# Kernel tuning notes

Measured on AMD Instinct MI355X. Metric: run time of the kernel, lower is better.

The kernel has to match this reference:

```python
import jax, jax.numpy as jnp
import numpy as np

N_NODES, N_EDGES, NNZ = 10000, 4000, 30000
IN_CH, HEADS, OUT_CH = 128, 2, 64


def _scale2_pattern(node, edge, num_nodes, num_edges):
    """Sparsity pattern of H @ (H^T H) where H is the node x edge incidence.
    Mirrors torch.sparse.mm + coalesce + (values > 0) mask (pattern only,
    since all values are positive sums of ones)."""
    # unique incidence pattern (coalesce)
    uk = np.unique(node.astype(np.int64) * num_edges + edge.astype(np.int64))
    n_u, e_u = uk // num_edges, uk % num_edges
    # --- stage 1: pattern of H^T H = edge pairs sharing a node ---
    order = np.argsort(n_u, kind="stable")
    ns, es = n_u[order], e_u[order]
    _, starts, cnts = np.unique(ns, return_index=True, return_counts=True)
    cpe = np.repeat(cnts, cnts)          # group size per sorted entry
    gpe = np.repeat(starts, cnts)        # group start per sorted entry
    tot = int(cpe.sum())
    within = np.arange(tot) - np.repeat(np.cumsum(cpe) - cpe, cpe)
    pe = np.repeat(es, cpe)
    pep = es[np.repeat(gpe, cpe) + within]
    pk = np.unique(pe * num_edges + pep)
    pe, pep = pk // num_edges, pk % num_edges
    # --- stage 2: pattern of H @ (H^T H) ---
    po = np.argsort(pe, kind="stable")
    pe_s, pep_s = pe[po], pep[po]
    cnt_e = np.bincount(pe_s, minlength=num_edges)
    ptr = np.concatenate([np.zeros(1, np.int64), np.cumsum(cnt_e)])
    c2 = cnt_e[e_u]
    tot2 = int(c2.sum())
    within2 = np.arange(tot2) - np.repeat(np.cumsum(c2) - c2, c2)
    v2 = np.repeat(n_u, c2)
    ep2 = pep_s[ptr[e_u].repeat(c2) + within2]
    k2 = np.unique(v2 * num_edges + ep2)
    return k2 // num_edges, k2 % num_edges


def setup_inputs() -> dict:
    rng = np.random.default_rng(0)
    node1 = rng.integers(0, N_NODES, NNZ).astype(np.int64)
    edge1 = rng.integers(0, N_EDGES, NNZ).astype(np.int64)
    node2, edge2 = _scale2_pattern(node1, edge1, N_NODES, N_EDGES)

    key = jax.random.key(0)
    k = jax.random.split(key, 4)
    HO = HEADS * OUT_CH
    xav1 = (2.0 / (IN_CH + HO)) ** 0.5
    xavo = (2.0 / (HO + OUT_CH)) ** 0.5
    return {
        "x": jax.random.normal(k[0], (N_NODES, IN_CH), jnp.float32),
        "hyperedge_index1": jnp.asarray(np.stack([node1, edge1]), jnp.int32),
        "hyperedge_index2": jnp.asarray(np.stack([node2, edge2]), jnp.int32),
        "W1": jax.random.normal(k[1], (HO, IN_CH), jnp.float32) * xav1,
        "b1": jnp.zeros((HO,), jnp.float32),
        "W2": jax.random.normal(k[2], (HO, IN_CH), jnp.float32) * xav1,
        "b2": jnp.zeros((HO,), jnp.float32),
        "Wout": jax.random.normal(k[3], (OUT_CH, HO), jnp.float32) * xavo,
        "bout": jnp.zeros((OUT_CH,), jnp.float32),
        "num_edges": N_EDGES,
    }


def _hconv(x, W, b, node_idx, edge_idx, num_edges):
    num_nodes = x.shape[0]
    xt = x @ W.T + b                                  # [N, H*O]
    g = xt[node_idx]                                  # [nnz, H*O] gather
    esum = jax.ops.segment_sum(g, edge_idx, num_segments=num_edges)
    cnt = jax.ops.segment_sum(jnp.ones(edge_idx.shape, xt.dtype), edge_idx,
                              num_segments=num_edges)
    emean = esum / jnp.maximum(cnt, 1.0)[:, None]     # scatter_mean (0 if empty)
    return jax.ops.segment_sum(emean[edge_idx], node_idx,
                               num_segments=num_nodes)  # scatter_add


def reference(x, hyperedge_index1, hyperedge_index2, W1, b1, W2, b2, Wout, bout,
              num_edges):
    o1 = _hconv(x, W1, b1, hyperedge_index1[0], hyperedge_index1[1], num_edges)
    o2 = _hconv(x, W2, b2, hyperedge_index2[0], hyperedge_index2[1], num_edges)
    o = 0.5 * (o1 + o2)                               # mean over 2 scales
    return o @ Wout.T + bout                          # output_proj
```

## Files before the change

kernel.cpp:

```cpp
#include <hip/hip_runtime.h>
#include <hip/hip_bf16.h>

#define N_NODES 10000
#define N_EDGES 4000
#define IN_CH   128
#define HOC     128
#define OUT_CH  64
#define CHUNK   16384

#define G_GEMM  625
#define G_NPTR  40

__device__ __forceinline__ float bf2f(unsigned short u) {
    union { unsigned int i; float f; } v;
    v.i = ((unsigned int)u) << 16;
    return v.f;
}
__device__ __forceinline__ unsigned short f2bfu(float f) {
    union { __hip_bfloat16 h; unsigned short u; } v;
    v.h = __float2bfloat16(f);
    return v.u;
}

__device__ __forceinline__ void load8(const void* base, size_t eoff, int isf32,
                                      float o[8]) {
    if (isf32) {
        const float4* q = (const float4*)((const float*)base + eoff);
        float4 a = q[0], b = q[1];
        o[0]=a.x; o[1]=a.y; o[2]=a.z; o[3]=a.w;
        o[4]=b.x; o[5]=b.y; o[6]=b.z; o[7]=b.w;
    } else {
        uint4 v = *(const uint4*)((const unsigned short*)base + eoff);
        const unsigned short* pv = (const unsigned short*)&v;
#pragma unroll
        for (int q = 0; q < 8; q++) o[q] = bf2f(pv[q]);
    }
}

__device__ __forceinline__ float loadS(const void* base, int i, int isf32) {
    return isf32 ? ((const float*)base)[i] : bf2f(((const unsigned short*)base)[i]);
}

__device__ __forceinline__ int probe_isf32(const unsigned int* __restrict__ x) {
    const int lane = threadIdx.x & 63;
    unsigned int w0 = x[lane * 2], w1 = x[lane * 2 + 1];
    int h = 0, z = 0;
    {
        unsigned int lo = w0 & 0xFFFFu;
        if (lo == 0u) z++; else if (((lo >> 7) & 0xFF) >= 0x90u) h++;
        lo = w1 & 0xFFFFu;
        if (lo == 0u) z++; else if (((lo >> 7) & 0xFF) >= 0x90u) h++;
    }
    unsigned long long bh = __ballot(h > 0);
    unsigned long long bz = __ballot(z == 2);
    return (__popcll(bh) > 8 || __popcll(bz) > 50) ? 1 : 0;
}

__device__ __forceinline__ void add4(float acc[4], uint2 u) {
    acc[0] += bf2f((unsigned short)(u.x & 0xFFFFu));
    acc[1] += bf2f((unsigned short)(u.x >> 16));
    acc[2] += bf2f((unsigned short)(u.y & 0xFFFFu));
    acc[3] += bf2f((unsigned short)(u.y >> 16));
}

__global__ __launch_bounds__(256) void weff_zero(
    const void* __restrict__ Wout,
    const void* __restrict__ W1, const void* __restrict__ b1,
    const void* __restrict__ W2, const void* __restrict__ b2,
    float* __restrict__ weff1, float* __restrict__ beff1,
    float* __restrict__ weff2, float* __restrict__ beff2,
    int* __restrict__ cntz, int* __restrict__ fillz,
    const unsigned int* __restrict__ xprobe)
{
    const int b = blockIdx.x;
    if (b == 4) {
        for (int t = threadIdx.x; t < 18000; t += 256) cntz[t] = 0;
        for (int t = threadIdx.x; t < 14000; t += 256) fillz[t] = 0;
        return;
    }
    __shared__ float wsh[64][IN_CH];
    const int isf32 = probe_isf32(xprobe);

    if (b == 5) {
        float* bsh = &wsh[0][0];
        const int t = threadIdx.x;
        {
            const int s = t >> 7, h = t & 127;
            bsh[t] = loadS(s ? b2 : b1, h, isf32);
        }
        __syncthreads();
        if (t < 128) {
            const int s = t >> 6, o = t & 63;
            float a = 0.f;
#pragma unroll 4
            for (int r = 0; r < 16; r++) {
                float v[8];
                load8(Wout, (size_t)o * 128 + r * 8, isf32, v);
#pragma unroll
                for (int q = 0; q < 8; q++) a += v[q] * bsh[s * 128 + r * 8 + q];
            }
            (s ? beff2 : beff1)[o] = 0.5f * a;
        }
        return;
    }

    const int s  = b >> 1;
    const int oh = b & 1;
    const void* Ws = s ? W2 : W1;
    float* outW = s ? weff2 : weff1;
    const int o  = oh * 32 + (threadIdx.x >> 3);
    const int i0 = (threadIdx.x & 7) * 16;
    float acc[16];
#pragma unroll
    for (int k = 0; k < 16; k++) acc[k] = 0.f;

    for (int pass = 0; pass < 2; pass++) {
        if (pass) __syncthreads();
        for (int r = 0; r < 4; r++) {
            int idx = r * 2048 + threadIdx.x * 8;
            float v[8];
            load8(Ws, (size_t)pass * 8192 + idx, isf32, v);
            float* d = &wsh[0][0] + idx;
#pragma unroll
            for (int q = 0; q < 8; q++) d[q] = v[q];
        }
        float wrow[64];
#pragma unroll
        for (int r = 0; r < 8; r++) {
            float v[8];
            load8(Wout, (size_t)o * 128 + pass * 64 + r * 8, isf32, v);
#pragma unroll
            for (int q = 0; q < 8; q++) wrow[r * 8 + q] = v[q];
        }
        __syncthreads();
#pragma unroll 4
        for (int h = 0; h < 64; h++) {
            const float wo = wrow[h];
            const float* wr = &wsh[h][i0];
#pragma unroll
            for (int k = 0; k < 16; k++) acc[k] += wo * wr[k];
        }
    }
#pragma unroll
    for (int k = 0; k < 16; k++)
        outW[o * 128 + i0 + k] = 0.5f * acc[k];
}

__global__ __launch_bounds__(256) void prep(
    const void* __restrict__ x,
    const float* __restrict__ weff1, const float* __restrict__ beff1,
    const float* __restrict__ weff2, const float* __restrict__ beff2,
    unsigned short* __restrict__ xtP1b, unsigned short* __restrict__ xtP2b,
    const int* __restrict__ idx1, int nnz1,
    const int* __restrict__ idx2, int nnz2,
    int* __restrict__ nptr,
    int* __restrict__ bh, int* __restrict__ cnt2,
    int* __restrict__ cnt1e, int* __restrict__ cnt1n, int nblk)
{
    __shared__ __align__(16) char smem[40000];
    int b = blockIdx.x;

    if (b < nblk) {
        int* h = (int*)smem;
        for (int t = threadIdx.x; t < N_EDGES; t += 256) h[t] = 0;
        __syncthreads();
        const int lo = b * CHUNK;
        const int hi = min(nnz2, lo + CHUNK);
        for (int i = lo + threadIdx.x; i < hi; i += 256)
            atomicAdd(&h[idx2[nnz2 + i]], 1);
        __syncthreads();
        int* dst = bh + (size_t)b * N_EDGES;
        for (int t = threadIdx.x; t < N_EDGES; t += 256) {
            int v = h[t];
            dst[t] = v;
            if (v) atomicAdd(&cnt2[t], v);
        }
        return;
    }
    b -= nblk;

    if (b < 8) {
        const int isEdge = b < 4;
        const int bid = isEdge ? b : (b - 4);
        const int nb = isEdge ? N_EDGES : N_NODES;
        const int* src = isEdge ? (idx1 + nnz1) : idx1;
        int* dst = isEdge ? cnt1e : cnt1n;
        int* h = (int*)smem;
        for (int t = threadIdx.x; t < nb; t += 256) h[t] = 0;
        __syncthreads();
        for (int i = bid * 256 + threadIdx.x; i < nnz1; i += 4 * 256)
            atomicAdd(&h[src[i]], 1);
        __syncthreads();
        for (int t = threadIdx.x; t < nb; t += 256) {
            int v = h[t];
            if (v) atomicAdd(&dst[t], v);
        }
        return;
    }
    b -= 8;

    if (b < G_GEMM) {
        const int isf32 = probe_isf32((const unsigned int*)x);
        float (*xs)[IN_CH] = (float (*)[IN_CH])smem;
        const int n0 = b * 16;
        {
            float v[8];
            load8(x, (size_t)n0 * IN_CH + (size_t)threadIdx.x * 8, isf32, v);
            float* dst = &xs[0][0] + threadIdx.x * 8;
#pragma unroll
            for (int q = 0; q < 8; q++) dst[q] = v[q];
        }
        __syncthreads();

        const int g   = threadIdx.x >> 7;
        const int sel = (threadIdx.x >> 6) & 1;
        const int j   = threadIdx.x & 63;
        const float* WE = sel ? weff2 : weff1;
        const float* BE = sel ? beff2 : beff1;
        unsigned short* xtP = sel ? xtP2b : xtP1b;

        float acc[8];
#pragma unroll
        for (int m = 0; m < 8; m++) acc[m] = 0.f;

        const float4* Wr = (const float4*)(WE + (size_t)j * 128);
        for (int kk = 0; kk < 16; kk++) {
            float4 a = Wr[kk * 2], c = Wr[kk * 2 + 1];
            float w[8] = {a.x, a.y, a.z, a.w, c.x, c.y, c.z, c.w};
#pragma unroll
            for (int m = 0; m < 8; m++) {
                const float* xr = &xs[g * 8 + m][kk * 8];
                acc[m] += xr[0]*w[0] + xr[1]*w[1] + xr[2]*w[2] + xr[3]*w[3]
                        + xr[4]*w[4] + xr[5]*w[5] + xr[6]*w[6] + xr[7]*w[7];
            }
        }
        const float bias = BE[j];
#pragma unroll
        for (int m = 0; m < 8; m++)
            xtP[(size_t)(n0 + g * 8 + m) * 64 + j] = f2bfu(acc[m] + bias);
        return;
    }
    b -= G_GEMM;

    {
        int n = b * 256 + threadIdx.x;
        if (n > N_NODES) return;
        int lo = 0, hi = nnz2;
        while (lo < hi) { int mid = (lo + hi) >> 1; if (idx2[mid] < n) lo = mid + 1; else hi = mid; }
        nptr[n] = lo;
    }
}

__global__ __launch_bounds__(256) void scans3(
    const int* __restrict__ cnt2, int* __restrict__ ptr2,
    const int* __restrict__ cnt1e, int* __restrict__ ptr1e,
    const int* __restrict__ cnt1n, int* __restrict__ ptr1n)
{
    const int* cnt; int* ptr; int nb;
    if (blockIdx.x == 0)      { cnt = cnt2;  ptr = ptr2;  nb = N_EDGES; }
    else if (blockIdx.x == 1) { cnt = cnt1e; ptr = ptr1e; nb = N_EDGES; }
    else                      { cnt = cnt1n; ptr = ptr1n; nb = N_NODES; }
    __shared__ int part[256];
    const int t = threadIdx.x;
    const int K = (nb + 255) >> 8;
    const int base = t * K;
    int s = 0;
    for (int q = 0; q < K; q++) {
        int i = base + q;
        s += (i < nb) ? cnt[i] : 0;
    }
    part[t] = s;
    __syncthreads();
    for (int d = 1; d < 256; d <<= 1) {
        int v = (t >= d) ? part[t - d] : 0;
        __syncthreads();
        part[t] += v;
        __syncthreads();
    }
    int run = part[t] - s;
    for (int q = 0; q < K; q++) {
        int i = base + q;
        if (i < nb) { ptr[i] = run; run += cnt[i]; }
    }
    if (t == 255) ptr[nb] = part[255];
}

__global__ __launch_bounds__(256) void sb_fb(
    const int* __restrict__ ptr2, int* __restrict__ bh, int nblk,
    const int* __restrict__ idx1, int nnz1,
    const int* __restrict__ ptr1e, int* __restrict__ fill1e,
    unsigned short* __restrict__ nodelist1,
    const int* __restrict__ ptr1n, int* __restrict__ fill1n,
    unsigned short* __restrict__ edgelist1)
{
    int b = blockIdx.x;
    if (b < 16) {
        int e = b * 256 + threadIdx.x;
        if (e >= N_EDGES) return;
        int run = ptr2[e];
        int k = 0;
        for (; k + 8 <= nblk; k += 8) {
            int v[8];
#pragma unroll
            for (int q = 0; q < 8; q++)
                v[q] = bh[(size_t)(k + q) * N_EDGES + e];
#pragma unroll
            for (int q = 0; q < 8; q++) {
                bh[(size_t)(k + q) * N_EDGES + e] = run;
                run += v[q];
            }
        }
        for (; k < nblk; k++) {
            int i = k * N_EDGES + e;
            int t = bh[i];
            bh[i] = run;
            run += t;
        }
        return;
    }
    b -= 16;
    int i = b * 256 + threadIdx.x;
    if (i >= nnz1) return;
    int n = idx1[i];
    int e = idx1[nnz1 + i];
    int se = atomicAdd(&fill1e[e], 1);
    nodelist1[ptr1e[e] + se] = (unsigned short)n;
    int sn = atomicAdd(&fill1n[n], 1);
    edgelist1[ptr1n[n] + sn] = (unsigned short)e;
}

__global__ __launch_bounds__(1024) void place_entries(
    const int* __restrict__ idx, int nnz, const int* __restrict__ bh,
    unsigned short* __restrict__ nodelist)
{
    __shared__ int lh[N_EDGES];
    for (int t = threadIdx.x; t < N_EDGES; t += 1024) lh[t] = 0;
    __syncthreads();
    const int b = blockIdx.x;
    const int lo = b * CHUNK;
    const int hi = min(nnz, lo + CHUNK);
    const int* bhb = bh + (size_t)b * N_EDGES;
    for (int i = lo + threadIdx.x; i < hi; i += 1024) {
        int n = idx[i];
        int e = idx[nnz + i];
        int s = atomicAdd(&lh[e], 1);
        nodelist[bhb[e] + s] = (unsigned short)n;
    }
}

__global__ __launch_bounds__(256) void edge_gather(
    const unsigned short* __restrict__ nodelist2, const int* __restrict__ ptr2,
    const unsigned int* __restrict__ xtP2u, unsigned int* __restrict__ emean2b,
    const unsigned short* __restrict__ nodelist1, const int* __restrict__ ptr1e,
    const unsigned int* __restrict__ xtP1u, unsigned int* __restrict__ emean1b)
{
    int b = blockIdx.x;
    if (b < 1000) {
        const int lane = threadIdx.x & 63;
        const int sub  = lane >> 4;
        const int ch4  = lane & 15;
        const int e = b * 4 + (threadIdx.x >> 6);
        const int lo = ptr2[e], hi = ptr2[e + 1];
        const uint2* src2 = (const uint2*)xtP2u;
        float acc[4] = {0.f, 0.f, 0.f, 0.f};
        int i = lo;
        for (; i + 32 <= hi; i += 32) {
            int n[8]; uint2 u[8];
#pragma unroll
            for (int q = 0; q < 8; q++) n[q] = nodelist2[i + 4 * q + sub];
#pragma unroll
            for (int q = 0; q < 8; q++) u[q] = src2[(size_t)n[q] * 16 + ch4];
#pragma unroll
            for (int q = 0; q < 8; q++) add4(acc, u[q]);
        }
        for (; i < hi; i += 4) {
            if (i + sub < hi) {
                int n0 = nodelist2[i + sub];
                add4(acc, src2[(size_t)n0 * 16 + ch4]);
            }
        }
#pragma unroll
        for (int q = 0; q < 4; q++) {
            acc[q] += __shfl_xor(acc[q], 16);
            acc[q] += __shfl_xor(acc[q], 32);
        }
        if (sub == 0) {
            const float inv = 1.f / fmaxf((float)(hi - lo), 1.f);
            uint2 o;
            o.x = ((unsigned int)f2bfu(acc[1] * inv) << 16) | f2bfu(acc[0] * inv);
            o.y = ((unsigned int)f2bfu(acc[3] * inv) << 16) | f2bfu(acc[2] * inv);
            ((uint2*)emean2b)[(size_t)e * 16 + ch4] = o;
        }
        return;
    }
    b -= 1000;
    {
        const int lane = threadIdx.x & 31;
        const int e = b * 8 + (threadIdx.x >> 5);
        const int lo = ptr1e[e], hi = ptr1e[e + 1];
        float accx = 0.f, accy = 0.f;
        for (int base = lo; base < hi; base += 32) {
            const int m = min(32, hi - base);
            int vl = (base + lane < hi) ? (int)nodelist1[base + lane] : 0;
            int t = 0;
            for (; t + 7 < m; t += 8) {
                int nn[8]; unsigned int uu[8];
#pragma unroll
                for (int q = 0; q < 8; q++) nn[q] = __shfl(vl, t + q, 32);
#pragma unroll
                for (int q = 0; q < 8; q++) uu[q] = xtP1u[nn[q] * 32 + lane];
#pragma unroll
                for (int q = 0; q < 8; q++) {
                    accx += bf2f((unsigned short)(uu[q] & 0xFFFFu));
                    accy += bf2f((unsigned short)(uu[q] >> 16));
                }
            }
            for (; t < m; t++) {
                int n = __shfl(vl, t, 32);
                unsigned int u = xtP1u[n * 32 + lane];
                accx += bf2f((unsigned short)(u & 0xFFFFu));
                accy += bf2f((unsigned short)(u >> 16));
            }
        }
        const float inv = 1.f / fmaxf((float)(hi - lo), 1.f);
        emean1b[e * 32 + lane] =
            ((unsigned int)f2bfu(accy * inv) << 16) | f2bfu(accx * inv);
    }
}

__global__ __launch_bounds__(256) void node_final(
    const int* __restrict__ vals2, const int* __restrict__ nptr,
    const unsigned int* __restrict__ emean2b,
    const unsigned short* __restrict__ edgelist1, const int* __restrict__ ptr1n,
    const unsigned int* __restrict__ emean1b,
    const void* __restrict__ bout, void* __restrict__ out,
    const unsigned int* __restrict__ xprobe)
{
    const int isf32 = probe_isf32(xprobe);
    const int lane = threadIdx.x & 63;
    const int sub  = lane >> 4;
    const int ch4  = lane & 15;
    const int n = blockIdx.x * 4 + (threadIdx.x >> 6);
    float acc[4] = {0.f, 0.f, 0.f, 0.f};

    {
        const int lo = nptr[n], hi = nptr[n + 1];
        const uint2* src = (const uint2*)emean2b;
        int i = lo;
        for (; i + 32 <= hi; i += 32) {
            int e[8]; uint2 u[8];
#pragma unroll
            for (int q = 0; q < 8; q++) e[q] = vals2[i + 4 * q + sub];
#pragma unroll
            for (int q = 0; q < 8; q++) u[q] = src[(size_t)e[q] * 16 + ch4];
#pragma unroll
            for (int q = 0; q < 8; q++) add4(acc, u[q]);
        }
        for (; i < hi; i += 4) {
            if (i + sub < hi)
                add4(acc, src[(size_t)vals2[i + sub] * 16 + ch4]);
        }
    }
    {
        const int lo = ptr1n[n], hi = ptr1n[n + 1];
        const uint2* src = (const uint2*)emean1b;
        int i = lo;
        for (; i + 32 <= hi; i += 32) {
            int e[8]; uint2 u[8];
#pragma unroll
            for (int q = 0; q < 8; q++) e[q] = edgelist1[i + 4 * q + sub];
#pragma unroll
            for (int q = 0; q < 8; q++) u[q] = src[(size_t)e[q] * 16 + ch4];
#pragma unroll
            for (int q = 0; q < 8; q++) add4(acc, u[q]);
        }
        for (; i < hi; i += 4) {
            if (i + sub < hi)
                add4(acc, src[(size_t)edgelist1[i + sub] * 16 + ch4]);
        }
    }
#pragma unroll
    for (int q = 0; q < 4; q++) {
        acc[q] += __shfl_xor(acc[q], 16);
        acc[q] += __shfl_xor(acc[q], 32);
    }
    if (sub == 0) {
        float r[4];
#pragma unroll
        for (int q = 0; q < 4; q++)
            r[q] = acc[q] + loadS(bout, ch4 * 4 + q, isf32);
        if (isf32) {
            ((float4*)out)[(size_t)n * 16 + ch4] =
                make_float4(r[0], r[1], r[2], r[3]);
        } else {
            uint2 o;
            o.x = ((unsigned int)f2bfu(r[1]) << 16) | f2bfu(r[0]);
            o.y = ((unsigned int)f2bfu(r[3]) << 16) | f2bfu(r[2]);
            ((uint2*)out)[(size_t)n * 16 + ch4] = o;
        }
    }
}

extern "C" void kernel_launch(void* const* d_in, const int* in_sizes, int n_in,
                              void* d_out, int out_size, void* d_ws, size_t ws_size,
                              hipStream_t stream)
{
    const void* x  = d_in[0];
    const int* idx1 = (const int*)d_in[1];
    const int* idx2 = (const int*)d_in[2];
    const void* W1 = d_in[3];
    const void* b1 = d_in[4];
    const void* W2 = d_in[5];
    const void* b2 = d_in[6];
    const void* Wo = d_in[7];
    const void* bo = d_in[8];

    const int nnz1 = in_sizes[1] / 2;
    const int nnz2 = in_sizes[2] / 2;
    const int nblk = (nnz2 + CHUNK - 1) / CHUNK;

    float* ws = (float*)d_ws;
    unsigned short* xtP1b = (unsigned short*)ws;
    unsigned int*   xtP1u = (unsigned int*)xtP1b;
    unsigned short* xtP2b = (unsigned short*)(ws + 320000);
    unsigned int*   xtP2u = (unsigned int*)xtP2b;
    int*   fill1e = (int*)(ws + 1280000);
    int*   fill1n = (int*)(ws + 1284000);
    int* cnt2  = (int*)(ws + 1550000);
    int* cnt1e = (int*)(ws + 1554000);
    int* cnt1n = (int*)(ws + 1558000);
    int* ptr2  = (int*)(ws + 1568000);
    int* ptr1e = (int*)(ws + 1572004);
    int* ptr1n = (int*)(ws + 1576008);
    int* nptr  = (int*)(ws + 1586012);
    float* weff1 = ws + 1596016;
    float* weff2 = ws + 1604208;
    float* beff1 = ws + 1612400;
    float* beff2 = ws + 1612464;
    unsigned int* emean2b = (unsigned int*)(ws + 1612528);
    unsigned int* emean1b = (unsigned int*)(ws + 1740528);
    unsigned short* nodelist2 = (unsigned short*)(ws + 1868528);
    const size_t nl2u = ((size_t)nnz2 + 1) / 2;
    unsigned short* nodelist1 = (unsigned short*)(ws + 1868528 + nl2u);
    const size_t nl1u = ((size_t)nnz1 + 1) / 2;
    unsigned short* edgelist1 = (unsigned short*)(ws + 1868528 + nl2u + nl1u);
    const size_t bh_off = (1868528 + nl2u + 2 * nl1u + 7) & ~(size_t)7;
    int* bh = (int*)(ws + bh_off);

    weff_zero<<<6, 256, 0, stream>>>(Wo, W1, b1, W2, b2,
                                     weff1, beff1, weff2, beff2,
                                     cnt2, fill1e, (const unsigned int*)x);

    prep<<<nblk + 8 + G_GEMM + G_NPTR, 256, 0, stream>>>(
        x, weff1, beff1, weff2, beff2, xtP1b, xtP2b,
        idx1, nnz1, idx2, nnz2,
        nptr, bh, cnt2, cnt1e, cnt1n, nblk);

    scans3<<<3, 256, 0, stream>>>(cnt2, ptr2, cnt1e, ptr1e, cnt1n, ptr1n);

    sb_fb<<<16 + (nnz1 + 255) / 256, 256, 0, stream>>>(
        ptr2, bh, nblk, idx1, nnz1, ptr1e, fill1e, nodelist1,
        ptr1n, fill1n, edgelist1);

    place_entries<<<nblk, 1024, 0, stream>>>(idx2, nnz2, bh, nodelist2);

    edge_gather<<<1000 + N_EDGES / 8, 256, 0, stream>>>(
        nodelist2, ptr2, xtP2u, emean2b,
        nodelist1, ptr1e, xtP1u, emean1b);

    node_final<<<N_NODES / 4, 256, 0, stream>>>(
        idx2 + nnz2, nptr, emean2b, edgelist1, ptr1n, emean1b,
        bo, d_out, (const unsigned int*)x);
}
```

Baseline: 198.5 us.

## Replace per-block histogram CSR build with global atomic fill for scale-2

The scale-2 CSR construction no longer stores per-chunk edge histograms, scans them per edge and places entries in a separate kernel. Entries are now scattered directly with global atomic counters per edge, fused into the same launch as the scale-1 fill. This drops one kernel launch, the histogram writes and the column-wise scan. In exchange it uses many global atomics on 4000 counters for a large nnz2, which risks contention, and the node order inside each edge list becomes nondeterministic.

After: 220.1 us. +10.9%, slower.

```diff
diff --git a/kernel.cpp b/kernel.cpp
--- a/kernel.cpp
+++ b/kernel.cpp
@@ -4,8 +4,6 @@
 #define N_NODES 10000
 #define N_EDGES 4000
 #define IN_CH   128
-#define HOC     128
-#define OUT_CH  64
 #define CHUNK   16384
 
 #define G_GEMM  625
@@ -69,13 +67,14 @@
     const void* __restrict__ W2, const void* __restrict__ b2,
     float* __restrict__ weff1, float* __restrict__ beff1,
     float* __restrict__ weff2, float* __restrict__ beff2,
-    int* __restrict__ cntz, int* __restrict__ fillz,
+    int* __restrict__ cntz, int* __restrict__ fillz, int* __restrict__ f2z,
     const unsigned int* __restrict__ xprobe)
 {
     const int b = blockIdx.x;
     if (b == 4) {
         for (int t = threadIdx.x; t < 18000; t += 256) cntz[t] = 0;
         for (int t = threadIdx.x; t < 14000; t += 256) fillz[t] = 0;
+        for (int t = threadIdx.x; t < 4000;  t += 256) f2z[t] = 0;
         return;
     }
     __shared__ float wsh[64][IN_CH];
@@ -153,8 +152,7 @@
     unsigned short* __restrict__ xtP1b, unsigned short* __restrict__ xtP2b,
     const int* __restrict__ idx1, int nnz1,
     const int* __restrict__ idx2, int nnz2,
-    int* __restrict__ nptr,
-    int* __restrict__ bh, int* __restrict__ cnt2,
+    int* __restrict__ nptr, int* __restrict__ cnt2,
     int* __restrict__ cnt1e, int* __restrict__ cnt1n, int nblk)
 {
     __shared__ __align__(16) char smem[40000];
@@ -169,10 +167,8 @@
         for (int i = lo + threadIdx.x; i < hi; i += 256)
             atomicAdd(&h[idx2[nnz2 + i]], 1);
         __syncthreads();
-        int* dst = bh + (size_t)b * N_EDGES;
         for (int t = threadIdx.x; t < N_EDGES; t += 256) {
             int v = h[t];
-            dst[t] = v;
             if (v) atomicAdd(&cnt2[t], v);
         }
         return;
@@ -285,8 +281,10 @@
     if (t == 255) ptr[nb] = part[255];
 }
 
-__global__ __launch_bounds__(256) void sb_fb(
-    const int* __restrict__ ptr2, int* __restrict__ bh, int nblk,
+__global__ __launch_bounds__(256) void fill_all(
+    const int* __restrict__ idx2, int nnz2,
+    const int* __restrict__ ptr2, int* __restrict__ fill2e,
+    unsigned short* __restrict__ nodelist2, int F2,
     const int* __restrict__ idx1, int nnz1,
     const int* __restrict__ ptr1e, int* __restrict__ fill1e,
     unsigned short* __restrict__ nodelist1,
@@ -294,31 +292,16 @@
     unsigned short* __restrict__ edgelist1)
 {
     int b = blockIdx.x;
-    if (b < 16) {
-        int e = b * 256 + threadIdx.x;
-        if (e >= N_EDGES) return;
-        int run = ptr2[e];
-        int k = 0;
-        for (; k + 8 <= nblk; k += 8) {
-            int v[8];
-#pragma unroll
-            for (int q = 0; q < 8; q++)
-                v[q] = bh[(size_t)(k + q) * N_EDGES + e];
-#pragma unroll
-            for (int q = 0; q < 8; q++) {
-                bh[(size_t)(k + q) * N_EDGES + e] = run;
-                run += v[q];
-            }
-        }
-        for (; k < nblk; k++) {
-            int i = k * N_EDGES + e;
-            int t = bh[i];
-            bh[i] = run;
-            run += t;
-        }
-        return;
-    }
-    b -= 16;
+    if (b < F2) {
+        int i = b * 256 + threadIdx.x;
+        if (i >= nnz2) return;
+        int n = idx2[i];
+        int e = idx2[nnz2 + i];
+        int s = atomicAdd(&fill2e[e], 1);
+        nodelist2[ptr2[e] + s] = (unsigned short)n;
+        return;
+    }
+    b -= F2;
     int i = b * 256 + threadIdx.x;
     if (i >= nnz1) return;
     int n = idx1[i];
@@ -327,25 +310,6 @@
     nodelist1[ptr1e[e] + se] = (unsigned short)n;
     int sn = atomicAdd(&fill1n[n], 1);
     edgelist1[ptr1n[n] + sn] = (unsigned short)e;
-}
-
-__global__ __launch_bounds__(1024) void place_entries(
-    const int* __restrict__ idx, int nnz, const int* __restrict__ bh,
-    unsigned short* __restrict__ nodelist)
-{
-    __shared__ int lh[N_EDGES];
-    for (int t = threadIdx.x; t < N_EDGES; t += 1024) lh[t] = 0;
-    __syncthreads();
-    const int b = blockIdx.x;
-    const int lo = b * CHUNK;
-    const int hi = min(nnz, lo + CHUNK);
-    const int* bhb = bh + (size_t)b * N_EDGES;
-    for (int i = lo + threadIdx.x; i < hi; i += 1024) {
-        int n = idx[i];
-        int e = idx[nnz + i];
-        int s = atomicAdd(&lh[e], 1);
-        nodelist[bhb[e] + s] = (unsigned short)n;
-    }
 }
 
 __global__ __launch_bounds__(256) void edge_gather(
@@ -518,12 +482,15 @@
     const int nnz1 = in_sizes[1] / 2;
     const int nnz2 = in_sizes[2] / 2;
     const int nblk = (nnz2 + CHUNK - 1) / CHUNK;
+    const int F2 = (nnz2 + 255) / 256;
+    const int F1 = (nnz1 + 255) / 256;
 
     float* ws = (float*)d_ws;
     unsigned short* xtP1b = (unsigned short*)ws;
     unsigned int*   xtP1u = (unsigned int*)xtP1b;
     unsigned short* xtP2b = (unsigned short*)(ws + 320000);
     unsigned int*   xtP2u = (unsigned int*)xtP2b;
+    int* fill2e = (int*)(ws + 640000);
     int*   fill1e = (int*)(ws + 1280000);
     int*   fill1n = (int*)(ws + 1284000);
     int* cnt2  = (int*)(ws + 1550000);
@@ -544,25 +511,23 @@
     unsigned short* nodelist1 = (unsigned short*)(ws + 1868528 + nl2u);
     const size_t nl1u = ((size_t)nnz1 + 1) / 2;
     unsigned short* edgelist1 = (unsigned short*)(ws + 1868528 + nl2u + nl1u);
-    const size_t bh_off = (1868528 + nl2u + 2 * nl1u + 7) & ~(size_t)7;
-    int* bh = (int*)(ws + bh_off);
 
     weff_zero<<<6, 256, 0, stream>>>(Wo, W1, b1, W2, b2,
                                      weff1, beff1, weff2, beff2,
-                                     cnt2, fill1e, (const unsigned int*)x);
+                                     cnt2, fill1e, fill2e,
+                                     (const unsigned int*)x);
 
     prep<<<nblk + 8 + G_GEMM + G_NPTR, 256, 0, stream>>>(
         x, weff1, beff1, weff2, beff2, xtP1b, xtP2b,
         idx1, nnz1, idx2, nnz2,
-        nptr, bh, cnt2, cnt1e, cnt1n, nblk);
+        nptr, cnt2, cnt1e, cnt1n, nblk);
 
     scans3<<<3, 256, 0, stream>>>(cnt2, ptr2, cnt1e, ptr1e, cnt1n, ptr1n);
 
-    sb_fb<<<16 + (nnz1 + 255) / 256, 256, 0, stream>>>(
-        ptr2, bh, nblk, idx1, nnz1, ptr1e, fill1e, nodelist1,
+    fill_all<<<F2 + F1, 256, 0, stream>>>(
+        idx2, nnz2, ptr2, fill2e, nodelist2, F2,
+        idx1, nnz1, ptr1e, fill1e, nodelist1,
         ptr1n, fill1n, edgelist1);
-
-    place_entries<<<nblk, 1024, 0, stream>>>(idx2, nnz2, bh, nodelist2);
 
     edge_gather<<<1000 + N_EDGES / 8, 256, 0, stream>>>(
         nodelist2, ptr2, xtP2u, emean2b,
```
